# Kernel tuning notes

Measured on AMD Instinct MI355X. Metric: run time of the kernel, lower is better.

Reference implementation:

```python
import jax, jax.numpy as jnp
import numpy as np

DIM = 256
NUM_HEADS = 8


def setup_inputs() -> dict:
    key = jax.random.key(0)
    ks = jax.random.split(key, 8)
    B, H, W = 2, 64, 64
    s = 0.02
    return {
        "query": jax.random.normal(ks[0], (B, H, W, DIM), jnp.float32),
        "sim": jax.random.normal(ks[1], (B, H, W, DIM), jnp.float32),
        "Wq": jax.random.normal(ks[2], (DIM, DIM), jnp.float32) * s,
        "bq": jnp.zeros((DIM,), jnp.float32),
        "Wkv": jax.random.normal(ks[3], (DIM, 2 * DIM), jnp.float32) * s,
        "bkv": jnp.zeros((2 * DIM,), jnp.float32),
        "Wp": jax.random.normal(ks[4], (DIM, DIM), jnp.float32) * s,
        "bp": jnp.zeros((DIM,), jnp.float32),
    }


def reference(query, sim, Wq, bq, Wkv, bkv, Wp, bp):
    B, H, W, dim = query.shape
    nh = NUM_HEADS
    dh = dim // nh
    scale = dh ** (-0.5)
    S = H * W

    # projections
    q = (query.reshape(B, S, dim) @ Wq + bq).reshape(B, S, nh, dh)
    kv = (sim.reshape(B, S, dim) @ Wkv + bkv).reshape(B, S, 2, nh, dh)
    k = kv[:, :, 0]  # [B,S,nh,dh]
    v = kv[:, :, 1]

    # attention: scores [B,nh,S,S]
    attn = jnp.einsum('bqhd,bkhd->bhqk', q * scale, k)
    attn = jax.nn.softmax(attn, axis=-1)
    x = jnp.einsum('bhqk,bkhd->bqhd', attn, v)  # [B,S,nh,dh]
    x = x.reshape(B, H, W, dim)
    return x @ Wp + bp
```

## Files before the change

kernel.cpp:

```cpp
#include <hip/hip_runtime.h>
#include <hip/hip_bf16.h>
#include <math.h>


#define SCALE 0.17677669529663687f
#define LOG2E 1.4426950408889634f

typedef __attribute__((ext_vector_type(8))) short short8;
typedef __attribute__((ext_vector_type(8))) _Float16 half8;
typedef __attribute__((ext_vector_type(4))) float f32x4;

static __device__ __forceinline__ unsigned short f2bf(float x) {
    union { float f; unsigned int u; } v; v.f = x;
    unsigned int r = v.u + 0x7fff + ((v.u >> 16) & 1);
    return (unsigned short)(r >> 16);
}
static __device__ __forceinline__ float bf2f(unsigned short h) {
    union { unsigned int u; float f; } v; v.u = ((unsigned int)h) << 16;
    return v.f;
}
static __device__ __forceinline__ float fexp2(float x) {
#if __has_builtin(__builtin_amdgcn_exp2f)
    return __builtin_amdgcn_exp2f(x);
#else
    float r; asm("v_exp_f32 %0, %1" : "=v"(r) : "v"(x)); return r;
#endif
}
static __device__ __forceinline__ unsigned int pk_bf16(float a, float b) {
    unsigned int r;
    asm("v_cvt_pk_bf16_f32 %0, %1, %2" : "=v"(r) : "v"(a), "v"(b));
    return r;
}
static __device__ __forceinline__ unsigned short f2h(float x) {
    _Float16 h = (_Float16)x;
    union { _Float16 h; unsigned short s; } u; u.h = h;
    return u.s;
}
static __device__ __forceinline__ float h2f(unsigned short s) {
    union { _Float16 h; unsigned short s; } u; u.s = s;
    return (float)u.h;
}

__global__ __launch_bounds__(256) void prep(
    const float* __restrict__ Wq, const float* __restrict__ Wkv,
    const float* __restrict__ Wp, unsigned short* __restrict__ wfp)
{
    __shared__ float T[64][68];
    const int bb = blockIdx.x, t = threadIdx.x;
    const int mat = bb >> 4, tile = bb & 15;
    const int kr0 = (tile >> 2) * 64;
    const int nc0 = (tile & 3) * 64;
    const float* src; int ldw, cb; float sc = 1.f;
    if (mat == 0)      { src = Wq;  ldw = 256; cb = 0;   sc = SCALE * LOG2E; }
    else if (mat == 1) { src = Wkv; ldw = 512; cb = 0;   }
    else if (mat == 2) { src = Wkv; ldw = 512; cb = 256; }
    else               { src = Wp;  ldw = 256; cb = 0;   }
    {
        const int rl = t >> 4, c4 = (t & 15) * 4;
#pragma unroll
        for (int rr = 0; rr < 4; ++rr) {
            float4 v = *(const float4*)&src[(long long)(kr0 + rr * 16 + rl) * ldw + cb + nc0 + c4];
            T[rr * 16 + rl][c4 + 0] = v.x; T[rr * 16 + rl][c4 + 1] = v.y;
            T[rr * 16 + rl][c4 + 2] = v.z; T[rr * 16 + rl][c4 + 3] = v.w;
        }
    }
    __syncthreads();
    {
        const int nl = t >> 2, kl0 = (t & 3) * 16;
        const long long orow = (long long)(mat * 256 + nc0 + nl) * 256 + kr0 + kl0;
        union { unsigned short s[16]; uint4 u[2]; } ph;
#pragma unroll
        for (int j = 0; j < 16; ++j)
            ph.s[j] = f2h(T[kl0 + j][nl] * sc);
        *(uint4*)&wfp[orow] = ph.u[0];
        *(uint4*)&wfp[orow + 8] = ph.u[1];
    }
}

__global__ __launch_bounds__(256) void gemm_qkv(
    const float* __restrict__ query, const float* __restrict__ sim,
    const unsigned short* __restrict__ wfp,
    const float* __restrict__ bq, const float* __restrict__ bkv,
    unsigned short* __restrict__ qbuf, unsigned short* __restrict__ kbuf,
    unsigned short* __restrict__ vTb)
{
    __shared__ unsigned short Xs[64 * 40], Ws[64 * 40];

    const int t = threadIdx.x, wave = t >> 6, lane = t & 63;
    const int col = lane & 15, quad = lane >> 4;
    const int by = blockIdx.y;
    const int kind = by >> 2;
    const int n0 = (by & 3) * 64;
    const int m0 = blockIdx.x * 64;
    const float* __restrict__ X = (kind == 0) ? query : sim;
    const int wrow0 = kind * 256 + n0;
    const int srow = t >> 2, spart = (t & 3) * 8;

    const f32x4 zero = {0.f, 0.f, 0.f, 0.f};
    f32x4 acc[4] = {zero, zero, zero, zero};

    for (int kt = 0; kt < 8; ++kt) {
        const int k0 = kt * 32;
        const float* xp = &X[(long long)(m0 + srow) * 256 + k0 + spart];
        float4 xa = *(const float4*)xp;
        float4 xb = *(const float4*)(xp + 4);
        float xv[8] = {xa.x, xa.y, xa.z, xa.w, xb.x, xb.y, xb.z, xb.w};
        union { unsigned short s[8]; uint4 u; } ph;
#pragma unroll
        for (int j = 0; j < 8; ++j) ph.s[j] = f2h(xv[j]);
        uint4 wh = *(const uint4*)&wfp[(long long)(wrow0 + srow) * 256 + k0 + spart];
        __syncthreads();
        *(uint4*)&Xs[srow * 40 + spart] = ph.u;
        *(uint4*)&Ws[srow * 40 + spart] = wh;
        __syncthreads();

        if (kind < 2) {
            half8 a = *(const half8*)(Xs + (wave * 16 + col) * 40 + quad * 8);
#pragma unroll
            for (int nt = 0; nt < 4; ++nt) {
                half8 b = *(const half8*)(Ws + (nt * 16 + col) * 40 + quad * 8);
                acc[nt] = __builtin_amdgcn_mfma_f32_16x16x32_f16(a, b, acc[nt], 0, 0, 0);
            }
        } else {
            half8 a = *(const half8*)(Ws + (wave * 16 + col) * 40 + quad * 8);
#pragma unroll
            for (int nt = 0; nt < 4; ++nt) {
                half8 b = *(const half8*)(Xs + (nt * 16 + col) * 40 + quad * 8);
                acc[nt] = __builtin_amdgcn_mfma_f32_16x16x32_f16(a, b, acc[nt], 0, 0, 0);
            }
        }
    }

    if (kind == 0) {
#pragma unroll
        for (int nt = 0; nt < 4; ++nt) {
            int n = n0 + nt * 16 + col;
            int h = n >> 5, d = n & 31;
            float bias = bq[n] * (SCALE * LOG2E);
#pragma unroll
            for (int r = 0; r < 4; ++r) {
                int mg = m0 + wave * 16 + quad * 4 + r;
                int b = mg >> 12, sidx = mg & 4095;
                qbuf[((long long)(b * 8 + h) * 4096 + sidx) * 32 + d] = f2bf(acc[nt][r] + bias);
            }
        }
    } else if (kind == 1) {
#pragma unroll
        for (int nt = 0; nt < 4; ++nt) {
            int n = n0 + nt * 16 + col;
            int h = n >> 5, d = n & 31;
            float bias = bkv[n];
#pragma unroll
            for (int r = 0; r < 4; ++r) {
                int mg = m0 + wave * 16 + quad * 4 + r;
                int b = mg >> 12, sidx = mg & 4095;
                kbuf[((long long)(b * 8 + h) * 4096 + sidx) * 32 + d] = f2bf(acc[nt][r] + bias);
            }
        }
    } else {
#pragma unroll
        for (int nt = 0; nt < 4; ++nt) {
            int s = m0 + nt * 16 + col;
            int b = s >> 12, sidx = s & 4095;
#pragma unroll
            for (int r = 0; r < 4; ++r) {
                int dcol = n0 + wave * 16 + quad * 4 + r;
                int h = dcol >> 5, dd = dcol & 31;
                float bias = bkv[256 + dcol];
                vTb[((long long)((b * 8 + h) * 32 + dd)) * 4096 + sidx] = f2bf(acc[nt][r] + bias);
            }
        }
    }
}

__global__ __launch_bounds__(256) void flash_mfma(
    const unsigned short* __restrict__ qbuf,
    const unsigned short* __restrict__ kbuf,
    const unsigned short* __restrict__ vT,
    float* __restrict__ xpart, float* __restrict__ lpart)
{
    __shared__ unsigned short Ks[128 * 40];
    __shared__ unsigned short Vt[32 * 152];
    __shared__ unsigned short Pb[8][640];

    const int t = threadIdx.x;
    const int wave = t >> 6, lane = t & 63;
    const int col = lane & 15, quad = lane >> 4;
    const int qb = blockIdx.x & 31;
    const int bh = (blockIdx.x >> 5) & 15;
    const int ks = blockIdx.x >> 9;
    const int q0 = qb * 128 + wave * 32;
    const long long kvbase = (long long)bh * 4096 * 32;
    unsigned short* pb0 = Pb[wave * 2];
    unsigned short* pb1 = Pb[wave * 2 + 1];

    const short8 qf0 = *(const short8*)(qbuf + kvbase + (long long)(q0 + col) * 32 + quad * 8);
    const short8 qf1 = *(const short8*)(qbuf + kvbase + (long long)(q0 + 16 + col) * 32 + quad * 8);

    const f32x4 zero = {0.f, 0.f, 0.f, 0.f};
    f32x4 o00 = zero, o01 = zero, o10 = zero, o11 = zero;
    float l0 = 0.f, l1 = 0.f;

    const int krow = t >> 2, kpart = (t & 3) * 8;
    const int vrow = t >> 4, vpart = (t & 15) * 8;

    for (int kt0 = 0; kt0 < 16; ++kt0) {
        const int kt = ks * 16 + kt0;
        uint4 kg0 = *(const uint4*)(kbuf + kvbase + (long long)(kt * 128 + krow) * 32 + kpart);
        uint4 kg1 = *(const uint4*)(kbuf + kvbase + (long long)(kt * 128 + krow + 64) * 32 + kpart);
        uint4 vg0 = *(const uint4*)(vT + ((long long)(bh * 32 + vrow)) * 4096 + kt * 128 + vpart);
        uint4 vg1 = *(const uint4*)(vT + ((long long)(bh * 32 + vrow + 16)) * 4096 + kt * 128 + vpart);
        __syncthreads();
        *(uint4*)(Ks + krow * 40 + kpart) = kg0;
        *(uint4*)(Ks + (krow + 64) * 40 + kpart) = kg1;
        *(uint4*)(Vt + vrow * 152 + vpart) = vg0;
        *(uint4*)(Vt + (vrow + 16) * 152 + vpart) = vg1;
        __syncthreads();

#pragma unroll
        for (int sb = 0; sb < 4; ++sb) {
            const int kb = sb * 32;
            short8 a0 = *(const short8*)(Ks + (kb + col) * 40 + quad * 8);
            short8 a1 = *(const short8*)(Ks + (kb + 16 + col) * 40 + quad * 8);
            short8 v0 = *(const short8*)(Vt + col * 152 + kb + quad * 8);
            short8 v1 = *(const short8*)(Vt + (16 + col) * 152 + kb + quad * 8);
            {
                f32x4 c0 = __builtin_amdgcn_mfma_f32_16x16x32_bf16(a0, qf0, zero, 0, 0, 0);
                f32x4 c1 = __builtin_amdgcn_mfma_f32_16x16x32_bf16(a1, qf0, zero, 0, 0, 0);
                float p0 = fexp2(c0[0]), p1 = fexp2(c0[1]), p2 = fexp2(c0[2]), p3 = fexp2(c0[3]);
                float p4 = fexp2(c1[0]), p5 = fexp2(c1[1]), p6 = fexp2(c1[2]), p7 = fexp2(c1[3]);
                l0 += ((p0 + p1) + (p2 + p3)) + ((p4 + p5) + (p6 + p7));
                uint2 w0 = make_uint2(pk_bf16(p0, p1), pk_bf16(p2, p3));
                uint2 w1 = make_uint2(pk_bf16(p4, p5), pk_bf16(p6, p7));
                *(uint2*)(pb0 + col * 40 + quad * 4) = w0;
                *(uint2*)(pb0 + col * 40 + 16 + quad * 4) = w1;
                short8 pf = *(const short8*)(pb0 + col * 40 + quad * 8);
                o00 = __builtin_amdgcn_mfma_f32_16x16x32_bf16(v0, pf, o00, 0, 0, 0);
                o01 = __builtin_amdgcn_mfma_f32_16x16x32_bf16(v1, pf, o01, 0, 0, 0);
            }
            {
                f32x4 c0 = __builtin_amdgcn_mfma_f32_16x16x32_bf16(a0, qf1, zero, 0, 0, 0);
                f32x4 c1 = __builtin_amdgcn_mfma_f32_16x16x32_bf16(a1, qf1, zero, 0, 0, 0);
                float p0 = fexp2(c0[0]), p1 = fexp2(c0[1]), p2 = fexp2(c0[2]), p3 = fexp2(c0[3]);
                float p4 = fexp2(c1[0]), p5 = fexp2(c1[1]), p6 = fexp2(c1[2]), p7 = fexp2(c1[3]);
                l1 += ((p0 + p1) + (p2 + p3)) + ((p4 + p5) + (p6 + p7));
                uint2 w0 = make_uint2(pk_bf16(p0, p1), pk_bf16(p2, p3));
                uint2 w1 = make_uint2(pk_bf16(p4, p5), pk_bf16(p6, p7));
                *(uint2*)(pb1 + col * 40 + quad * 4) = w0;
                *(uint2*)(pb1 + col * 40 + 16 + quad * 4) = w1;
                short8 pf = *(const short8*)(pb1 + col * 40 + quad * 8);
                o10 = __builtin_amdgcn_mfma_f32_16x16x32_bf16(v0, pf, o10, 0, 0, 0);
                o11 = __builtin_amdgcn_mfma_f32_16x16x32_bf16(v1, pf, o11, 0, 0, 0);
            }
        }
    }

    l0 += __shfl_xor(l0, 16, 64); l0 += __shfl_xor(l0, 32, 64);
    l1 += __shfl_xor(l1, 16, 64); l1 += __shfl_xor(l1, 32, 64);

    const int b = bh >> 3, hh = bh & 7;
    float* xp = xpart + (long long)ks * 2097152;
    float* r0p = xp + ((long long)(b * 4096 + q0 + col)) * 256 + hh * 32;
    *(float4*)(r0p + quad * 4)      = make_float4(o00[0], o00[1], o00[2], o00[3]);
    *(float4*)(r0p + 16 + quad * 4) = make_float4(o01[0], o01[1], o01[2], o01[3]);
    float* r1p = xp + ((long long)(b * 4096 + q0 + 16 + col)) * 256 + hh * 32;
    *(float4*)(r1p + quad * 4)      = make_float4(o10[0], o10[1], o10[2], o10[3]);
    *(float4*)(r1p + 16 + quad * 4) = make_float4(o11[0], o11[1], o11[2], o11[3]);

    if (quad == 0)      lpart[ks * 65536 + bh * 4096 + q0 + col] = l0;
    else if (quad == 1) lpart[ks * 65536 + bh * 4096 + q0 + 16 + col] = l1;
}

__global__ __launch_bounds__(256) void gemm_outp(
    const float* __restrict__ xpart, const float* __restrict__ lpart,
    const unsigned short* __restrict__ wfp,
    const float* __restrict__ bp, float* __restrict__ out)
{
    __shared__ unsigned short XsH[64 * 40], XsL[64 * 40], Ws[64 * 40];

    const int t = threadIdx.x, wave = t >> 6, lane = t & 63;
    const int col = lane & 15, quad = lane >> 4;
    const int n0 = blockIdx.y * 64;
    const int m0 = blockIdx.x * 64;
    const int wrow0 = 768 + n0;
    const int srow = t >> 2, spart = (t & 3) * 8;
    const int r = m0 + srow;
    const int bidx = r >> 12, s = r & 4095;
    const float* __restrict__ xa = xpart;
    const float* __restrict__ xb = xpart + 2097152;

    const f32x4 zero = {0.f, 0.f, 0.f, 0.f};
    f32x4 acc[4] = {zero, zero, zero, zero};

    for (int kt = 0; kt < 8; ++kt) {
        const int k0 = kt * 32;
        const int head = k0 >> 5;
        float la = lpart[(bidx * 8 + head) * 4096 + s];
        float lb = lpart[65536 + (bidx * 8 + head) * 4096 + s];
        float linv = 1.f / (la + lb);
        const float* pa = &xa[(long long)r * 256 + k0 + spart];
        const float* pb = &xb[(long long)r * 256 + k0 + spart];
        float4 a0 = *(const float4*)pa, a1 = *(const float4*)(pa + 4);
        float4 b0 = *(const float4*)pb, b1 = *(const float4*)(pb + 4);
        float xv[8] = {(a0.x + b0.x) * linv, (a0.y + b0.y) * linv,
                       (a0.z + b0.z) * linv, (a0.w + b0.w) * linv,
                       (a1.x + b1.x) * linv, (a1.y + b1.y) * linv,
                       (a1.z + b1.z) * linv, (a1.w + b1.w) * linv};
        union { unsigned short s4[8]; uint4 u; } ph, pl;
#pragma unroll
        for (int j = 0; j < 8; ++j) {
            unsigned short h = f2h(xv[j]);
            ph.s4[j] = h;
            pl.s4[j] = f2h(xv[j] - h2f(h));
        }
        uint4 wh = *(const uint4*)&wfp[(long long)(wrow0 + srow) * 256 + k0 + spart];
        __syncthreads();
        *(uint4*)&XsH[srow * 40 + spart] = ph.u;
        *(uint4*)&XsL[srow * 40 + spart] = pl.u;
        *(uint4*)&Ws[srow * 40 + spart] = wh;
        __syncthreads();

        half8 a_h = *(const half8*)(XsH + (wave * 16 + col) * 40 + quad * 8);
        half8 a_l = *(const half8*)(XsL + (wave * 16 + col) * 40 + quad * 8);
#pragma unroll
        for (int nt = 0; nt < 4; ++nt) {
            half8 b = *(const half8*)(Ws + (nt * 16 + col) * 40 + quad * 8);
            acc[nt] = __builtin_amdgcn_mfma_f32_16x16x32_f16(a_h, b, acc[nt], 0, 0, 0);
            acc[nt] = __builtin_amdgcn_mfma_f32_16x16x32_f16(a_l, b, acc[nt], 0, 0, 0);
        }
    }

#pragma unroll
    for (int nt = 0; nt < 4; ++nt) {
        int n = n0 + nt * 16 + col;
        float bias = bp[n];
#pragma unroll
        for (int rr = 0; rr < 4; ++rr) {
            int mg = m0 + wave * 16 + quad * 4 + rr;
            out[(long long)mg * 256 + n] = acc[nt][rr] + bias;
        }
    }
}

extern "C" void kernel_launch(void* const* d_in, const int* in_sizes, int n_in,
                              void* d_out, int out_size, void* d_ws, size_t ws_size,
                              hipStream_t stream) {
    const float* query = (const float*)d_in[0];
    const float* sim   = (const float*)d_in[1];
    const float* Wq    = (const float*)d_in[2];
    const float* bq    = (const float*)d_in[3];
    const float* Wkv   = (const float*)d_in[4];
    const float* bkv   = (const float*)d_in[5];
    const float* Wp    = (const float*)d_in[6];
    const float* bp    = (const float*)d_in[7];
    float* out = (float*)d_out;

    unsigned short* wsb = (unsigned short*)d_ws;
    unsigned short* qbuf = wsb;
    unsigned short* kbuf = wsb + 2097152;
    unsigned short* vT   = wsb + 4194304;
    unsigned short* wfp  = wsb + 6291456;
    float* xpart = (float*)(wsb + 6553600);
    float* lpart = (float*)(wsb + 14942208);

    prep      <<<dim3(64),      256, 0, stream>>>(Wq, Wkv, Wp, wfp);
    gemm_qkv  <<<dim3(128, 12), 256, 0, stream>>>(query, sim, wfp, bq, bkv,
                                                  qbuf, kbuf, vT);
    flash_mfma<<<dim3(1024),    256, 0, stream>>>(qbuf, kbuf, vT, xpart, lpart);
    gemm_outp <<<dim3(128, 4),  256, 0, stream>>>(xpart, lpart, wfp, bp, out);
}
```

Measured before the change: 158.9 us.

## Split attention KV into four partitions with fp16 partials; preload weights in GEMMs

```diff
diff --git a/kernel.cpp b/kernel.cpp
--- a/kernel.cpp
+++ b/kernel.cpp
@@ -14,10 +14,6 @@
     union { float f; unsigned int u; } v; v.f = x;
     unsigned int r = v.u + 0x7fff + ((v.u >> 16) & 1);
     return (unsigned short)(r >> 16);
-}
-static __device__ __forceinline__ float bf2f(unsigned short h) {
-    union { unsigned int u; float f; } v; v.u = ((unsigned int)h) << 16;
-    return v.f;
 }
 static __device__ __forceinline__ float fexp2(float x) {
 #if __has_builtin(__builtin_amdgcn_exp2f)
@@ -84,7 +80,7 @@
     unsigned short* __restrict__ qbuf, unsigned short* __restrict__ kbuf,
     unsigned short* __restrict__ vTb)
 {
-    __shared__ unsigned short Xs[64 * 40], Ws[64 * 40];
+    __shared__ unsigned short Ws[64 * 264];
 
     const int t = threadIdx.x, wave = t >> 6, lane = t & 63;
     const int col = lane & 15, quad = lane >> 4;
@@ -94,38 +90,43 @@
     const int m0 = blockIdx.x * 64;
     const float* __restrict__ X = (kind == 0) ? query : sim;
     const int wrow0 = kind * 256 + n0;
-    const int srow = t >> 2, spart = (t & 3) * 8;
+
+    {
+        const int r = t >> 2, seg = (t & 3) * 64;
+#pragma unroll
+        for (int j = 0; j < 8; ++j) {
+            uint4 w = *(const uint4*)&wfp[(long long)(wrow0 + r) * 256 + seg + j * 8];
+            *(uint4*)&Ws[r * 264 + seg + j * 8] = w;
+        }
+    }
+    __syncthreads();
 
     const f32x4 zero = {0.f, 0.f, 0.f, 0.f};
     f32x4 acc[4] = {zero, zero, zero, zero};
 
+#pragma unroll
     for (int kt = 0; kt < 8; ++kt) {
         const int k0 = kt * 32;
-        const float* xp = &X[(long long)(m0 + srow) * 256 + k0 + spart];
-        float4 xa = *(const float4*)xp;
-        float4 xb = *(const float4*)(xp + 4);
-        float xv[8] = {xa.x, xa.y, xa.z, xa.w, xb.x, xb.y, xb.z, xb.w};
-        union { unsigned short s[8]; uint4 u; } ph;
-#pragma unroll
-        for (int j = 0; j < 8; ++j) ph.s[j] = f2h(xv[j]);
-        uint4 wh = *(const uint4*)&wfp[(long long)(wrow0 + srow) * 256 + k0 + spart];
-        __syncthreads();
-        *(uint4*)&Xs[srow * 40 + spart] = ph.u;
-        *(uint4*)&Ws[srow * 40 + spart] = wh;
-        __syncthreads();
-
         if (kind < 2) {
-            half8 a = *(const half8*)(Xs + (wave * 16 + col) * 40 + quad * 8);
+            const float* xp = &X[(long long)(m0 + wave * 16 + col) * 256 + k0 + quad * 8];
+            float4 xa = *(const float4*)xp;
+            float4 xb = *(const float4*)(xp + 4);
+            half8 a = {(_Float16)xa.x, (_Float16)xa.y, (_Float16)xa.z, (_Float16)xa.w,
+                       (_Float16)xb.x, (_Float16)xb.y, (_Float16)xb.z, (_Float16)xb.w};
 #pragma unroll
             for (int nt = 0; nt < 4; ++nt) {
-                half8 b = *(const half8*)(Ws + (nt * 16 + col) * 40 + quad * 8);
+                half8 b = *(const half8*)(Ws + (nt * 16 + col) * 264 + k0 + quad * 8);
                 acc[nt] = __builtin_amdgcn_mfma_f32_16x16x32_f16(a, b, acc[nt], 0, 0, 0);
             }
         } else {
-            half8 a = *(const half8*)(Ws + (wave * 16 + col) * 40 + quad * 8);
+            half8 a = *(const half8*)(Ws + (wave * 16 + col) * 264 + k0 + quad * 8);
 #pragma unroll
             for (int nt = 0; nt < 4; ++nt) {
-                half8 b = *(const half8*)(Xs + (nt * 16 + col) * 40 + quad * 8);
+                const float* xp = &X[(long long)(m0 + nt * 16 + col) * 256 + k0 + quad * 8];
+                float4 xa = *(const float4*)xp;
+                float4 xb = *(const float4*)(xp + 4);
+                half8 b = {(_Float16)xa.x, (_Float16)xa.y, (_Float16)xa.z, (_Float16)xa.w,
+                           (_Float16)xb.x, (_Float16)xb.y, (_Float16)xb.z, (_Float16)xb.w};
                 acc[nt] = __builtin_amdgcn_mfma_f32_16x16x32_f16(a, b, acc[nt], 0, 0, 0);
             }
         }
@@ -177,7 +178,7 @@
     const unsigned short* __restrict__ qbuf,
     const unsigned short* __restrict__ kbuf,
     const unsigned short* __restrict__ vT,
-    float* __restrict__ xpart, float* __restrict__ lpart)
+    unsigned short* __restrict__ xpart, float* __restrict__ lpart)
 {
     __shared__ unsigned short Ks[128 * 40];
     __shared__ unsigned short Vt[32 * 152];
@@ -204,8 +205,8 @@
     const int krow = t >> 2, kpart = (t & 3) * 8;
     const int vrow = t >> 4, vpart = (t & 15) * 8;
 
-    for (int kt0 = 0; kt0 < 16; ++kt0) {
-        const int kt = ks * 16 + kt0;
+    for (int kt0 = 0; kt0 < 8; ++kt0) {
+        const int kt = ks * 8 + kt0;
         uint4 kg0 = *(const uint4*)(kbuf + kvbase + (long long)(kt * 128 + krow) * 32 + kpart);
         uint4 kg1 = *(const uint4*)(kbuf + kvbase + (long long)(kt * 128 + krow + 64) * 32 + kpart);
         uint4 vg0 = *(const uint4*)(vT + ((long long)(bh * 32 + vrow)) * 4096 + kt * 128 + vpart);
@@ -259,72 +260,85 @@
     l1 += __shfl_xor(l1, 16, 64); l1 += __shfl_xor(l1, 32, 64);
 
     const int b = bh >> 3, hh = bh & 7;
-    float* xp = xpart + (long long)ks * 2097152;
-    float* r0p = xp + ((long long)(b * 4096 + q0 + col)) * 256 + hh * 32;
-    *(float4*)(r0p + quad * 4)      = make_float4(o00[0], o00[1], o00[2], o00[3]);
-    *(float4*)(r0p + 16 + quad * 4) = make_float4(o01[0], o01[1], o01[2], o01[3]);
-    float* r1p = xp + ((long long)(b * 4096 + q0 + 16 + col)) * 256 + hh * 32;
-    *(float4*)(r1p + quad * 4)      = make_float4(o10[0], o10[1], o10[2], o10[3]);
-    *(float4*)(r1p + 16 + quad * 4) = make_float4(o11[0], o11[1], o11[2], o11[3]);
+    unsigned short* xp = xpart + (long long)ks * 2097152;
+    {
+        unsigned short* rp = xp + ((long long)(b * 4096 + q0 + col)) * 256 + hh * 32;
+        union { unsigned short s[4]; uint2 u; } pa, pb2;
+#pragma unroll
+        for (int r = 0; r < 4; ++r) { pa.s[r] = f2h(o00[r]); pb2.s[r] = f2h(o01[r]); }
+        *(uint2*)(rp + quad * 4) = pa.u;
+        *(uint2*)(rp + 16 + quad * 4) = pb2.u;
+    }
+    {
+        unsigned short* rp = xp + ((long long)(b * 4096 + q0 + 16 + col)) * 256 + hh * 32;
+        union { unsigned short s[4]; uint2 u; } pa, pb2;
+#pragma unroll
+        for (int r = 0; r < 4; ++r) { pa.s[r] = f2h(o10[r]); pb2.s[r] = f2h(o11[r]); }
+        *(uint2*)(rp + quad * 4) = pa.u;
+        *(uint2*)(rp + 16 + quad * 4) = pb2.u;
+    }
 
     if (quad == 0)      lpart[ks * 65536 + bh * 4096 + q0 + col] = l0;
     else if (quad == 1) lpart[ks * 65536 + bh * 4096 + q0 + 16 + col] = l1;
 }
 
 __global__ __launch_bounds__(256) void gemm_outp(
-    const float* __restrict__ xpart, const float* __restrict__ lpart,
+    const unsigned short* __restrict__ xpart, const float* __restrict__ lpart,
     const unsigned short* __restrict__ wfp,
     const float* __restrict__ bp, float* __restrict__ out)
 {
-    __shared__ unsigned short XsH[64 * 40], XsL[64 * 40], Ws[64 * 40];
+    __shared__ unsigned short Ws[64 * 264];
 
     const int t = threadIdx.x, wave = t >> 6, lane = t & 63;
     const int col = lane & 15, quad = lane >> 4;
     const int n0 = blockIdx.y * 64;
     const int m0 = blockIdx.x * 64;
     const int wrow0 = 768 + n0;
-    const int srow = t >> 2, spart = (t & 3) * 8;
-    const int r = m0 + srow;
-    const int bidx = r >> 12, s = r & 4095;
-    const float* __restrict__ xa = xpart;
-    const float* __restrict__ xb = xpart + 2097152;
+
+    {
+        const int r = t >> 2, seg = (t & 3) * 64;
+#pragma unroll
+        for (int j = 0; j < 8; ++j) {
+            uint4 w = *(const uint4*)&wfp[(long long)(wrow0 + r) * 256 + seg + j * 8];
+            *(uint4*)&Ws[r * 264 + seg + j * 8] = w;
+        }
+    }
+    __syncthreads();
+
+    const int row = m0 + wave * 16 + col;
+    const int bidx = row >> 12, sr = row & 4095;
 
     const f32x4 zero = {0.f, 0.f, 0.f, 0.f};
     f32x4 acc[4] = {zero, zero, zero, zero};
 
+#pragma unroll
     for (int kt = 0; kt < 8; ++kt) {
         const int k0 = kt * 32;
-        const int head = k0 >> 5;
-        float la = lpart[(bidx * 8 + head) * 4096 + s];
-        float lb = lpart[65536 + (bidx * 8 + head) * 4096 + s];
-        float linv = 1.f / (la + lb);
-        const float* pa = &xa[(long long)r * 256 + k0 + spart];
-        const float* pb = &xb[(long long)r * 256 + k0 + spart];
-        float4 a0 = *(const float4*)pa, a1 = *(const float4*)(pa + 4);
-        float4 b0 = *(const float4*)pb, b1 = *(const float4*)(pb + 4);
-        float xv[8] = {(a0.x + b0.x) * linv, (a0.y + b0.y) * linv,
-                       (a0.z + b0.z) * linv, (a0.w + b0.w) * linv,
-                       (a1.x + b1.x) * linv, (a1.y + b1.y) * linv,
-                       (a1.z + b1.z) * linv, (a1.w + b1.w) * linv};
-        union { unsigned short s4[8]; uint4 u; } ph, pl;
+        float lsum = 0.f;
+#pragma unroll
+        for (int ss = 0; ss < 4; ++ss)
+            lsum += lpart[ss * 65536 + (bidx * 8 + kt) * 4096 + sr];
+        const float linv = 1.f / lsum;
+
+        union { unsigned short s[8]; uint4 u; } p[4];
+#pragma unroll
+        for (int ss = 0; ss < 4; ++ss)
+            p[ss].u = *(const uint4*)&xpart[(long long)ss * 2097152 +
+                                            (long long)row * 256 + k0 + quad * 8];
+        _Float16 ah[8], al[8];
 #pragma unroll
         for (int j = 0; j < 8; ++j) {
-            unsigned short h = f2h(xv[j]);
-            ph.s4[j] = h;
-            pl.s4[j] = f2h(xv[j] - h2f(h));
-        }
-        uint4 wh = *(const uint4*)&wfp[(long long)(wrow0 + srow) * 256 + k0 + spart];
-        __syncthreads();
-        *(uint4*)&XsH[srow * 40 + spart] = ph.u;
-        *(uint4*)&XsL[srow * 40 + spart] = pl.u;
-        *(uint4*)&Ws[srow * 40 + spart] = wh;
-        __syncthreads();
-
-        half8 a_h = *(const half8*)(XsH + (wave * 16 + col) * 40 + quad * 8);
-        half8 a_l = *(const half8*)(XsL + (wave * 16 + col) * 40 + quad * 8);
+            float xv = (h2f(p[0].s[j]) + h2f(p[1].s[j]) +
+                        h2f(p[2].s[j]) + h2f(p[3].s[j])) * linv;
+            _Float16 h = (_Float16)xv;
+            ah[j] = h;
+            al[j] = (_Float16)(xv - (float)h);
+        }
+        half8 a_h = {ah[0], ah[1], ah[2], ah[3], ah[4], ah[5], ah[6], ah[7]};
+        half8 a_l = {al[0], al[1], al[2], al[3], al[4], al[5], al[6], al[7]};
 #pragma unroll
         for (int nt = 0; nt < 4; ++nt) {
-            half8 b = *(const half8*)(Ws + (nt * 16 + col) * 40 + quad * 8);
+            half8 b = *(const half8*)(Ws + (nt * 16 + col) * 264 + k0 + quad * 8);
             acc[nt] = __builtin_amdgcn_mfma_f32_16x16x32_f16(a_h, b, acc[nt], 0, 0, 0);
             acc[nt] = __builtin_amdgcn_mfma_f32_16x16x32_f16(a_l, b, acc[nt], 0, 0, 0);
         }
@@ -360,12 +374,12 @@
     unsigned short* kbuf = wsb + 2097152;
     unsigned short* vT   = wsb + 4194304;
     unsigned short* wfp  = wsb + 6291456;
-    float* xpart = (float*)(wsb + 6553600);
+    unsigned short* xpart = wsb + 6553600;
     float* lpart = (float*)(wsb + 14942208);
 
     prep      <<<dim3(64),      256, 0, stream>>>(Wq, Wkv, Wp, wfp);
     gemm_qkv  <<<dim3(128, 12), 256, 0, stream>>>(query, sim, wfp, bq, bkv,
                                                   qbuf, kbuf, vT);
-    flash_mfma<<<dim3(1024),    256, 0, stream>>>(qbuf, kbuf, vT, xpart, lpart);
+    flash_mfma<<<dim3(2048),    256, 0, stream>>>(qbuf, kbuf, vT, xpart, lpart);
     gemm_outp <<<dim3(128, 4),  256, 0, stream>>>(xpart, lpart, wfp, bp, out);
 }
```

After: 182.4 us. +14.8%, slower.

## Split flash attention KV range four ways and store partials in fp16

Applied to the files above, without the earlier changes.

```diff
diff --git a/kernel.cpp b/kernel.cpp
--- a/kernel.cpp
+++ b/kernel.cpp
@@ -14,10 +14,6 @@
     union { float f; unsigned int u; } v; v.f = x;
     unsigned int r = v.u + 0x7fff + ((v.u >> 16) & 1);
     return (unsigned short)(r >> 16);
-}
-static __device__ __forceinline__ float bf2f(unsigned short h) {
-    union { unsigned int u; float f; } v; v.u = ((unsigned int)h) << 16;
-    return v.f;
 }
 static __device__ __forceinline__ float fexp2(float x) {
 #if __has_builtin(__builtin_amdgcn_exp2f)
@@ -177,7 +173,7 @@
     const unsigned short* __restrict__ qbuf,
     const unsigned short* __restrict__ kbuf,
     const unsigned short* __restrict__ vT,
-    float* __restrict__ xpart, float* __restrict__ lpart)
+    unsigned short* __restrict__ xpart, float* __restrict__ lpart)
 {
     __shared__ unsigned short Ks[128 * 40];
     __shared__ unsigned short Vt[32 * 152];
@@ -204,8 +200,8 @@
     const int krow = t >> 2, kpart = (t & 3) * 8;
     const int vrow = t >> 4, vpart = (t & 15) * 8;
 
-    for (int kt0 = 0; kt0 < 16; ++kt0) {
-        const int kt = ks * 16 + kt0;
+    for (int kt0 = 0; kt0 < 8; ++kt0) {
+        const int kt = ks * 8 + kt0;
         uint4 kg0 = *(const uint4*)(kbuf + kvbase + (long long)(kt * 128 + krow) * 32 + kpart);
         uint4 kg1 = *(const uint4*)(kbuf + kvbase + (long long)(kt * 128 + krow + 64) * 32 + kpart);
         uint4 vg0 = *(const uint4*)(vT + ((long long)(bh * 32 + vrow)) * 4096 + kt * 128 + vpart);
@@ -259,20 +255,30 @@
     l1 += __shfl_xor(l1, 16, 64); l1 += __shfl_xor(l1, 32, 64);
 
     const int b = bh >> 3, hh = bh & 7;
-    float* xp = xpart + (long long)ks * 2097152;
-    float* r0p = xp + ((long long)(b * 4096 + q0 + col)) * 256 + hh * 32;
-    *(float4*)(r0p + quad * 4)      = make_float4(o00[0], o00[1], o00[2], o00[3]);
-    *(float4*)(r0p + 16 + quad * 4) = make_float4(o01[0], o01[1], o01[2], o01[3]);
-    float* r1p = xp + ((long long)(b * 4096 + q0 + 16 + col)) * 256 + hh * 32;
-    *(float4*)(r1p + quad * 4)      = make_float4(o10[0], o10[1], o10[2], o10[3]);
-    *(float4*)(r1p + 16 + quad * 4) = make_float4(o11[0], o11[1], o11[2], o11[3]);
+    unsigned short* xp = xpart + (long long)ks * 2097152;
+    {
+        unsigned short* rp = xp + ((long long)(b * 4096 + q0 + col)) * 256 + hh * 32;
+        union { unsigned short s[4]; uint2 u; } pa, pb2;
+#pragma unroll
+        for (int r = 0; r < 4; ++r) { pa.s[r] = f2h(o00[r]); pb2.s[r] = f2h(o01[r]); }
+        *(uint2*)(rp + quad * 4) = pa.u;
+        *(uint2*)(rp + 16 + quad * 4) = pb2.u;
+    }
+    {
+        unsigned short* rp = xp + ((long long)(b * 4096 + q0 + 16 + col)) * 256 + hh * 32;
+        union { unsigned short s[4]; uint2 u; } pa, pb2;
+#pragma unroll
+        for (int r = 0; r < 4; ++r) { pa.s[r] = f2h(o10[r]); pb2.s[r] = f2h(o11[r]); }
+        *(uint2*)(rp + quad * 4) = pa.u;
+        *(uint2*)(rp + 16 + quad * 4) = pb2.u;
+    }
 
     if (quad == 0)      lpart[ks * 65536 + bh * 4096 + q0 + col] = l0;
     else if (quad == 1) lpart[ks * 65536 + bh * 4096 + q0 + 16 + col] = l1;
 }
 
 __global__ __launch_bounds__(256) void gemm_outp(
-    const float* __restrict__ xpart, const float* __restrict__ lpart,
+    const unsigned short* __restrict__ xpart, const float* __restrict__ lpart,
     const unsigned short* __restrict__ wfp,
     const float* __restrict__ bp, float* __restrict__ out)
 {
@@ -286,32 +292,31 @@
     const int srow = t >> 2, spart = (t & 3) * 8;
     const int r = m0 + srow;
     const int bidx = r >> 12, s = r & 4095;
-    const float* __restrict__ xa = xpart;
-    const float* __restrict__ xb = xpart + 2097152;
 
     const f32x4 zero = {0.f, 0.f, 0.f, 0.f};
     f32x4 acc[4] = {zero, zero, zero, zero};
 
     for (int kt = 0; kt < 8; ++kt) {
         const int k0 = kt * 32;
-        const int head = k0 >> 5;
-        float la = lpart[(bidx * 8 + head) * 4096 + s];
-        float lb = lpart[65536 + (bidx * 8 + head) * 4096 + s];
-        float linv = 1.f / (la + lb);
-        const float* pa = &xa[(long long)r * 256 + k0 + spart];
-        const float* pb = &xb[(long long)r * 256 + k0 + spart];
-        float4 a0 = *(const float4*)pa, a1 = *(const float4*)(pa + 4);
-        float4 b0 = *(const float4*)pb, b1 = *(const float4*)(pb + 4);
-        float xv[8] = {(a0.x + b0.x) * linv, (a0.y + b0.y) * linv,
-                       (a0.z + b0.z) * linv, (a0.w + b0.w) * linv,
-                       (a1.x + b1.x) * linv, (a1.y + b1.y) * linv,
-                       (a1.z + b1.z) * linv, (a1.w + b1.w) * linv};
+        float lsum = lpart[(bidx * 8 + kt) * 4096 + s]
+                   + lpart[65536 + (bidx * 8 + kt) * 4096 + s]
+                   + lpart[131072 + (bidx * 8 + kt) * 4096 + s]
+                   + lpart[196608 + (bidx * 8 + kt) * 4096 + s];
+        const float linv = 1.f / lsum;
+
+        union { unsigned short s4[8]; uint4 u; } p[4];
+#pragma unroll
+        for (int ss = 0; ss < 4; ++ss)
+            p[ss].u = *(const uint4*)&xpart[(long long)ss * 2097152 +
+                                            (long long)r * 256 + k0 + spart];
         union { unsigned short s4[8]; uint4 u; } ph, pl;
 #pragma unroll
         for (int j = 0; j < 8; ++j) {
-            unsigned short h = f2h(xv[j]);
+            float xv = (h2f(p[0].s4[j]) + h2f(p[1].s4[j]) +
+                        h2f(p[2].s4[j]) + h2f(p[3].s4[j])) * linv;
+            unsigned short h = f2h(xv);
             ph.s4[j] = h;
-            pl.s4[j] = f2h(xv[j] - h2f(h));
+            pl.s4[j] = f2h(xv - h2f(h));
         }
         uint4 wh = *(const uint4*)&wfp[(long long)(wrow0 + srow) * 256 + k0 + spart];
         __syncthreads();
@@ -360,12 +365,12 @@
     unsigned short* kbuf = wsb + 2097152;
     unsigned short* vT   = wsb + 4194304;
     unsigned short* wfp  = wsb + 6291456;
-    float* xpart = (float*)(wsb + 6553600);
+    unsigned short* xpart = wsb + 6553600;
     float* lpart = (float*)(wsb + 14942208);
 
     prep      <<<dim3(64),      256, 0, stream>>>(Wq, Wkv, Wp, wfp);
     gemm_qkv  <<<dim3(128, 12), 256, 0, stream>>>(query, sim, wfp, bq, bkv,
                                                   qbuf, kbuf, vT);
-    flash_mfma<<<dim3(1024),    256, 0, stream>>>(qbuf, kbuf, vT, xpart, lpart);
+    flash_mfma<<<dim3(2048),    256, 0, stream>>>(qbuf, kbuf, vT, xpart, lpart);
     gemm_outp <<<dim3(128, 4),  256, 0, stream>>>(xpart, lpart, wfp, bp, out);
 }
```

Result: no change. 156.0 us (-1.8%).
